# Kernel optimization log

Hardware: AMD Instinct MI355X
Metric: run time of the kernel (lower is better)

Reference implementation:

```python
import jax, jax.numpy as jnp
import numpy as np

N_WIRES = 10
N_BLOCKS = 4
BATCH = 8192
FEAT = 4 * N_WIRES
DIM = 2 ** N_WIRES
BN_EPS = 1e-5

# sign of PauliZ on wire i for each basis state index (wire 0 = most significant bit,
# matching torchquantum's [bsz, 2, 2, ..., 2] state layout)
_k = np.arange(DIM)
_bits = (_k[None, :] >> (N_WIRES - 1 - np.arange(N_WIRES))[:, None]) & 1
SIGNS = jnp.asarray(1.0 - 2.0 * _bits, dtype=jnp.float32)  # [n_wires, 2^n]

H_GATE = jnp.array([[1, 1], [1, -1]], dtype=jnp.complex64) * jnp.complex64(0.70710678)
SX_GATE = jnp.complex64(0.5) * jnp.array([[1 + 1j, 1 - 1j], [1 - 1j, 1 + 1j]], dtype=jnp.complex64)


def rx_mat(theta):
    t = jnp.asarray(theta) * 0.5
    c = jnp.cos(t).astype(jnp.complex64)
    s = (-1j) * jnp.sin(t).astype(jnp.complex64)
    return jnp.stack([jnp.stack([c, s], -1), jnp.stack([s, c], -1)], -2)


def ry_mat(theta):
    t = jnp.asarray(theta) * 0.5
    c = jnp.cos(t).astype(jnp.complex64)
    s = jnp.sin(t).astype(jnp.complex64)
    return jnp.stack([jnp.stack([c, -s], -1), jnp.stack([s, c], -1)], -2)


def rz_mat(theta):
    e = jnp.exp(jnp.complex64(-0.5j) * jnp.asarray(theta).astype(jnp.complex64))
    z = jnp.zeros_like(e)
    return jnp.stack([jnp.stack([e, z], -1), jnp.stack([z, jnp.conj(e)], -1)], -2)


def apply_1q(state, gate, wire):
    # state: [B, 2, 2, ..., 2]; gate: [2,2] (shared) or [B,2,2] (per-sample encoder)
    s = jnp.moveaxis(state, wire + 1, -1)
    if gate.ndim == 3:
        s = jnp.einsum('bij,b...j->b...i', gate, s)
    else:
        s = jnp.einsum('ij,b...j->b...i', gate, s)
    return jnp.moveaxis(s, -1, wire + 1)


def apply_cnot(state, c, t):
    s = jnp.moveaxis(state, (c + 1, t + 1), (-2, -1))  # [..., ctrl, tgt]
    s = jnp.stack([s[..., 0, :], s[..., 1, ::-1]], axis=-2)
    return jnp.moveaxis(s, (-2, -1), (c + 1, t + 1))


def measure_all_z(state):
    probs = (state.real ** 2 + state.imag ** 2).reshape(state.shape[0], -1)  # [B, 2^n]
    return probs @ SIGNS.T  # [B, n_wires]


def encode(state, feats):
    # GeneralEncoder: per wire i apply rx, ry, rz, rx with data angles feats[:, 4i..4i+3]
    for i in range(N_WIRES):
        state = apply_1q(state, rx_mat(feats[:, 4 * i]), i)
        state = apply_1q(state, ry_mat(feats[:, 4 * i + 1]), i)
        state = apply_1q(state, rz_mat(feats[:, 4 * i + 2]), i)
        state = apply_1q(state, rx_mat(feats[:, 4 * i + 3]), i)
    return state


def qnn(feats, rz1, ry1, rz2, rz3):
    B = feats.shape[0]
    state = jnp.zeros((B, DIM), jnp.complex64).at[:, 0].set(1.0)
    state = state.reshape((B,) + (2,) * N_WIRES)
    for k in range(N_BLOCKS):
        for i in range(N_WIRES):
            state = apply_1q(state, rz_mat(rz1[k, i]), i)
        for i in range(N_WIRES):
            state = apply_1q(state, ry_mat(ry1[k, i]), i)
        for i in range(N_WIRES):
            state = apply_1q(state, rz_mat(rz2[k, i]), i)
        for i in range(N_WIRES):  # circular CNOT ring
            state = apply_cnot(state, i, (i + 1) % N_WIRES)
        if k != N_BLOCKS - 1:
            state = encode(state, feats)
    outs = [measure_all_z(state)]
    for i in range(N_WIRES):
        state = apply_1q(state, H_GATE, i)
    outs.append(measure_all_z(state))
    for i in range(N_WIRES):
        state = apply_1q(state, H_GATE, i)
        state = apply_1q(state, SX_GATE, i)
    outs.append(measure_all_z(state))
    for i in range(N_WIRES):  # only the last rz3 layer is applied in the source
        state = apply_1q(state, rz_mat(rz3[-1, i]), i)
    outs.append(measure_all_z(state))
    return jnp.concatenate(outs, axis=-1)  # [B, 4*n_wires]


def setup_inputs() -> dict:
    key = jax.random.key(0)
    ks = jax.random.split(key, 13)
    pi = np.float32(np.pi)
    w_scale = 1.0 / np.sqrt(np.float32(FEAT))
    return {
        'x': jax.random.normal(ks[0], (BATCH, FEAT), jnp.float32),
        'qlin_w': jax.random.normal(ks[1], (FEAT, FEAT), jnp.float32) * w_scale,
        'qlin_b': jax.random.normal(ks[2], (FEAT,), jnp.float32) * w_scale,
        'bn_gamma': jnp.ones((FEAT,), jnp.float32),
        'bn_beta': jnp.zeros((FEAT,), jnp.float32),
        'clin_w': jax.random.normal(ks[3], (FEAT, FEAT), jnp.float32) * w_scale,
        'clin_b': jax.random.normal(ks[4], (FEAT,), jnp.float32) * w_scale,
        'lin_w': jax.random.normal(ks[5], (FEAT, 2 * FEAT), jnp.float32) * w_scale,
        'lin_b': jax.random.normal(ks[6], (FEAT,), jnp.float32) * w_scale,
        'rz1': jax.random.uniform(ks[7], (N_BLOCKS, N_WIRES), jnp.float32, -pi, pi),
        'ry1': jax.random.uniform(ks[8], (N_BLOCKS, N_WIRES), jnp.float32, -pi, pi),
        'rz2': jax.random.uniform(ks[9], (N_BLOCKS, N_WIRES), jnp.float32, -pi, pi),
        'rz3': jax.random.uniform(ks[10], (N_BLOCKS, N_WIRES), jnp.float32, -pi, pi),
    }


def reference(x, qlin_w, qlin_b, bn_gamma, bn_beta, clin_w, clin_b, lin_w, lin_b, rz1, ry1, rz2, rz3):
    # quantum branch: Linear -> BatchNorm1d (training-mode batch stats) -> QNN
    xq = x @ qlin_w.T + qlin_b
    mu = xq.mean(axis=0)
    var = ((xq - mu) ** 2).mean(axis=0)  # biased variance, as torch BN
    xq = (xq - mu) * jax.lax.rsqrt(var + BN_EPS) * bn_gamma + bn_beta
    x1 = qnn(xq, rz1, ry1, rz2, rz3)
    # classical branch
    x2 = jax.nn.relu(x @ clin_w.T + clin_b)
    return jnp.concatenate([x1, x2], axis=-1) @ lin_w.T + lin_b
```

## Files before the change

### kernel.cpp

```cpp
#include <hip/hip_runtime.h>
#include <math.h>


typedef float v2f __attribute__((ext_vector_type(2)));
typedef unsigned uiv2 __attribute__((ext_vector_type(2)));

__device__ __forceinline__ float bperm1(int addr, float v){
  return __int_as_float(__builtin_amdgcn_ds_bpermute(addr, __float_as_int(v)));
}
__device__ __forceinline__ v2f bperm2(int addr, v2f v){
  v2f r; r.x = bperm1(addr, v.x); r.y = bperm1(addr, v.y); return r;
}
__device__ __forceinline__ v2f vs(float x){ return (v2f){x,x}; }

template<int C>
__device__ __forceinline__ float dppf(float x){
  return __int_as_float(__builtin_amdgcn_update_dpp(0, __float_as_int(x),
                                                    C, 0xf, 0xf, true));
}
#define QP_X1 0xB1
#define QP_X2 0x4E

__device__ __forceinline__ float xor1f(float x, int ){ return dppf<QP_X1>(x); }
__device__ __forceinline__ float xor2f(float x, int ){ return dppf<QP_X2>(x); }

__device__ __forceinline__ float xor4f(float x, int ){
  return __int_as_float(__builtin_amdgcn_ds_swizzle(__float_as_int(x), 0x101F));
}
__device__ __forceinline__ float xor8f(float x, int ){
  return __int_as_float(__builtin_amdgcn_ds_swizzle(__float_as_int(x), 0x201F));
}

#if __has_builtin(__builtin_amdgcn_permlane16_swap) && __has_builtin(__builtin_amdgcn_permlane32_swap)
__device__ __forceinline__ float xor16f(float x, int lane){
  uiv2 r = __builtin_amdgcn_permlane16_swap(__float_as_uint(x), __float_as_uint(x),
                                            false, false);
  return __uint_as_float((lane & 16) ? r.x : r.y);
}
__device__ __forceinline__ float xor32f(float x, int lane){
  uiv2 r = __builtin_amdgcn_permlane32_swap(__float_as_uint(x), __float_as_uint(x),
                                            false, false);
  return __uint_as_float((lane & 32) ? r.x : r.y);
}
#else
__device__ __forceinline__ float xor16f(float x, int lane){ return bperm1((lane^16)<<2, x); }
__device__ __forceinline__ float xor32f(float x, int lane){ return bperm1((lane^32)<<2, x); }
#endif

#define DEF_XORV(NAME, F1) \
__device__ __forceinline__ v2f NAME(v2f v, int lane){ \
  v2f r; r.x = F1(v.x,lane); r.y = F1(v.y,lane); return r; }
DEF_XORV(xor1v,  xor1f)
DEF_XORV(xor2v,  xor2f)
DEF_XORV(xor4v,  xor4f)
DEF_XORV(xor8v,  xor8f)
DEF_XORV(xor16v, xor16f)
DEF_XORV(xor32v, xor32f)

__device__ __forceinline__ float dsum(float x){
  x += dppf<0x111>(x);
  x += dppf<0x112>(x);
  x += dppf<0x114>(x);
  x += dppf<0x118>(x);
  x += dppf<0x142>(x);
  x += dppf<0x143>(x);
  return x;
}


#define DEF_GCROSS(NAME, PFN) \
__device__ __forceinline__ void NAME(v2f (&R)[8], v2f (&I)[8], int lane, bool hi, \
                                     const float* g){ \
  const float gar = hi ? g[6] : g[0], gai = hi ? g[7] : g[1]; \
  const float gbr = hi ? g[4] : g[2], gbi = hi ? g[5] : g[3]; \
  const v2f A=vs(gar), B=vs(gai), C=vs(gbr), D=vs(gbi); \
  _Pragma("unroll") \
  for (int p=0;p<8;++p){ \
    v2f PR = PFN(R[p],lane); \
    v2f PI = PFN(I[p],lane); \
    v2f nr = A*R[p] - B*I[p] + C*PR - D*PI; \
    v2f ni = A*I[p] + B*R[p] + C*PI + D*PR; \
    R[p]=nr; I[p]=ni; } \
}
DEF_GCROSS(g_cross_x32, xor32v)
DEF_GCROSS(g_cross_x16, xor16v)
DEF_GCROSS(g_cross_x8,  xor8v)
DEF_GCROSS(g_cross_x4,  xor4v)
DEF_GCROSS(g_cross_x2,  xor2v)
DEF_GCROSS(g_cross_x1,  xor1v)

template<int PM>
__device__ __forceinline__ void g_localp(v2f (&R)[8], v2f (&I)[8], const float* g)
{
  const v2f g00r=vs(g[0]), g00i=vs(g[1]), g01r=vs(g[2]), g01i=vs(g[3]);
  const v2f g10r=vs(g[4]), g10i=vs(g[5]), g11r=vs(g[6]), g11i=vs(g[7]);
#pragma unroll
  for (int p=0;p<8;++p) if (!(p&PM)) {
    const int q = p|PM;
    v2f r0=R[p], i0=I[p], r1=R[q], i1=I[q];
    R[p] = g00r*r0 - g00i*i0 + g01r*r1 - g01i*i1;
    I[p] = g00r*i0 + g00i*r0 + g01r*i1 + g01i*r1;
    R[q] = g10r*r0 - g10i*i0 + g11r*r1 - g11i*i1;
    I[q] = g10r*i0 + g10i*r0 + g11r*i1 + g11i*r1;
  }
}

__device__ __forceinline__ void g_local9(v2f (&R)[8], v2f (&I)[8], const float* g)
{
  const v2f Gr0 = (v2f){g[0], g[4]};
  const v2f Gi0 = (v2f){g[1], g[5]};
  const v2f Gr1 = (v2f){g[2], g[6]};
  const v2f Gi1 = (v2f){g[3], g[7]};
#pragma unroll
  for (int p=0;p<8;++p) {
    v2f Rx = vs(R[p].x), Ix = vs(I[p].x);
    v2f Ry = vs(R[p].y), Iy = vs(I[p].y);
    R[p] = Gr0*Rx - Gi0*Ix + Gr1*Ry - Gi1*Iy;
    I[p] = Gr0*Ix + Gi0*Rx + Gr1*Iy + Gi1*Ry;
  }
}

__device__ __forceinline__ void cnot_ring(v2f (&R)[8], v2f (&I)[8],
                                          int addrg, int lane, bool c5)
{
#pragma unroll
  for (int p=0;p<8;++p) R[p] = bperm2(addrg, R[p]);
#pragma unroll
  for (int p=0;p<8;++p) I[p] = bperm2(addrg, I[p]);
#pragma unroll
  for (int p=0;p<4;++p) {
    v2f a=R[p], b=R[p|4];
    R[p]   = c5 ? b : a;
    R[p|4] = c5 ? a : b;
    v2f ai=I[p], bi=I[p|4];
    I[p]   = c5 ? bi : ai;
    I[p|4] = c5 ? ai : bi;
  }
#pragma unroll
  for (int p=0;p<8;++p) if ((p&4)&&!(p&2)) {
    const int q=p|2;
    v2f t=R[p]; R[p]=R[q]; R[q]=t;
    t=I[p]; I[p]=I[q]; I[q]=t;
  }
#pragma unroll
  for (int p=0;p<8;++p) if ((p&2)&&!(p&1)) {
    const int q=p|1;
    v2f t=R[p]; R[p]=R[q]; R[q]=t;
    t=I[p]; I[p]=I[q]; I[q]=t;
  }
#pragma unroll
  for (int p=1;p<8;p+=2) {
    R[p] = __builtin_shufflevector(R[p],R[p],1,0);
    I[p] = __builtin_shufflevector(I[p],I[p],1,0);
  }
#pragma unroll
  for (int p=0;p<8;++p) {
    R[p].y = xor32f(R[p].y, lane);
    I[p].y = xor32f(I[p].y, lane);
  }
}

__global__ __launch_bounds__(256) void k_pre(const float* __restrict__ x,
    const float* __restrict__ qw, const float* __restrict__ qb,
    float* __restrict__ ps)
{
  const int f = blockIdx.x >> 3, slice = blockIdx.x & 7;
  const int t = threadIdx.x;
  __shared__ float wf[40];
  __shared__ float a1[4], a2[4];
  if (t < 40) wf[t] = qw[f*40 + t];
  __syncthreads();
  const float bf = qb[f];
  float s1 = 0.f, s2 = 0.f;
#pragma unroll
  for (int i = 0; i < 4; ++i) {
    const int s = slice*1024 + t + i*256;
    const float4* xr = (const float4*)(x + s*40);
    float d = bf;
#pragma unroll
    for (int q = 0; q < 10; ++q) {
      float4 v = xr[q];
      d = fmaf(v.x, wf[4*q+0], d);
      d = fmaf(v.y, wf[4*q+1], d);
      d = fmaf(v.z, wf[4*q+2], d);
      d = fmaf(v.w, wf[4*q+3], d);
    }
    s1 += d; s2 = fmaf(d, d, s2);
  }
  s1 = dsum(s1); s2 = dsum(s2);
  const int lane = t & 63, wid = t >> 6;
  if (lane == 63) { a1[wid] = s1; a2[wid] = s2; }
  __syncthreads();
  if (t == 0) {
    ps[blockIdx.x*2+0] = a1[0]+a1[1]+a1[2]+a1[3];
    ps[blockIdx.x*2+1] = a2[0]+a2[1]+a2[2]+a2[3];
  }
}


#define GEN10(PTR) \
  g_cross_x32(R,I,lane,h0,(PTR)+0);  g_cross_x16(R,I,lane,h1,(PTR)+8);  \
  g_cross_x8 (R,I,lane,h2,(PTR)+16); g_cross_x4 (R,I,lane,h3,(PTR)+24); \
  g_cross_x2 (R,I,lane,h4,(PTR)+32); g_cross_x1 (R,I,lane,h5,(PTR)+40); \
  g_localp<4>(R,I,(PTR)+48);   g_localp<2>(R,I,(PTR)+56);   \
  g_localp<1>(R,I,(PTR)+64);   g_local9(R,I,(PTR)+72);

__global__ __launch_bounds__(256) void k_qnn(const float* __restrict__ x,
    const float* __restrict__ qlin_w, const float* __restrict__ qlin_b,
    const float* __restrict__ ps,
    const float* __restrict__ gamma, const float* __restrict__ beta,
    const float* __restrict__ rz1, const float* __restrict__ ry1,
    const float* __restrict__ rz2,
    const float* __restrict__ clin_w, const float* __restrict__ clin_b,
    const float* __restrict__ lin_w, const float* __restrict__ lin_b,
    float* __restrict__ out)
{
  const int tix  = threadIdx.x;
  const int lane = tix & 63;
  const int wv   = tix >> 6;

  __shared__ float Gbuf[40][8];
  __shared__ float bnA[40], bnC[40];
  __shared__ float Ebuf[4][10][8];
  __shared__ float Fbuf[4][3][10][8];
  __shared__ float xs [4][40];
  __shared__ float xqs[4][40];
  __shared__ float x1s[4][40];
  __shared__ float x2s[4][40];

  if (tix < 160) xs[tix/40][tix%40] = x[blockIdx.x*160 + tix];
  if (tix >= 160 && tix < 200) {
    const int gi = tix - 160;
    float g = rz1[gi], ay = ry1[gi], bz = rz2[gi];
    float ca, sa, cp, sp, cm, sm;
    sincosf(0.5f*ay, &sa, &ca);
    sincosf(0.5f*(bz+g), &sp, &cp);
    sincosf(0.5f*(bz-g), &sm, &cm);
    float* G = &Gbuf[gi][0];
    G[0]= ca*cp; G[1]=-ca*sp;
    G[2]=-sa*cm; G[3]= sa*sm;
    G[4]= sa*cm; G[5]= sa*sm;
    G[6]= ca*cp; G[7]= ca*sp;
  }
  if (tix >= 200 && tix < 240) {
    const int f = tix - 200;
    float s1 = 0.f, s2 = 0.f;
#pragma unroll
    for (int k = 0; k < 8; ++k) {
      s1 += ps[(f*8+k)*2+0];
      s2 += ps[(f*8+k)*2+1];
    }
    float mu  = s1 * (1.f/8192.f);
    float var = s2 * (1.f/8192.f) - mu*mu;
    float a = gamma[f] * rsqrtf(var + 1e-5f);
    bnA[f] = a; bnC[f] = beta[f] - mu*a;
  }
  __syncthreads();

  if (tix < 160) {
    const int sl = tix/40, f = tix - sl*40;
    const float4* qw = (const float4*)(qlin_w + f*40);
    float acc = qlin_b[f];
#pragma unroll
    for (int q = 0; q < 10; ++q) {
      float4 v = qw[q];
      acc = fmaf(v.x, xs[sl][4*q+0], acc);
      acc = fmaf(v.y, xs[sl][4*q+1], acc);
      acc = fmaf(v.z, xs[sl][4*q+2], acc);
      acc = fmaf(v.w, xs[sl][4*q+3], acc);
    }
    xqs[sl][f] = acc;
  }
  __syncthreads();

  if (lane < 10) {
    const int i = lane;
    const int f = 4*i;
    float h0 = 0.5f * fmaf(xqs[wv][f+0], bnA[f+0], bnC[f+0]);
    float h1 = 0.5f * fmaf(xqs[wv][f+1], bnA[f+1], bnC[f+1]);
    float h2 = 0.5f * fmaf(xqs[wv][f+2], bnA[f+2], bnC[f+2]);
    float h3 = 0.5f * fmaf(xqs[wv][f+3], bnA[f+3], bnC[f+3]);
    float c0,s0,c1,s1,c2,s2,c3,s3;
    sincosf(h0,&s0,&c0); sincosf(h1,&s1,&c1);
    sincosf(h2,&s2,&c2); sincosf(h3,&s3,&c3);
    float A00r=c1*c0, A00i= s1*s0;
    float A01r=-s1*c0, A01i=-c1*s0;
    float A10r= s1*c0, A10i=-c1*s0;
    float A11r= c1*c0, A11i=-s1*s0;
    float B00r = A00r*c2 + A00i*s2, B00i = A00i*c2 - A00r*s2;
    float B01r = A01r*c2 + A01i*s2, B01i = A01i*c2 - A01r*s2;
    float B10r = A10r*c2 - A10i*s2, B10i = A10i*c2 + A10r*s2;
    float B11r = A11r*c2 - A11i*s2, B11i = A11i*c2 + A11r*s2;
    float* e = &Ebuf[wv][i][0];
    e[0] = c3*B00r + s3*B10i;  e[1] = c3*B00i - s3*B10r;
    e[2] = c3*B01r + s3*B11i;  e[3] = c3*B01i - s3*B11r;
    e[4] = c3*B10r + s3*B00i;  e[5] = c3*B10i - s3*B00r;
    e[6] = c3*B11r + s3*B01i;  e[7] = c3*B11i - s3*B01r;
  }

  if (lane < 30) {
    const int k = lane/10, i = lane - k*10;
    const float* U = &Gbuf[(k+1)*10 + i][0];
    const float* E = &Ebuf[wv][i][0];
    float u00r=U[0],u00i=U[1],u01r=U[2],u01i=U[3],u10r=U[4],u10i=U[5],u11r=U[6],u11i=U[7];
    float e00r=E[0],e00i=E[1],e01r=E[2],e01i=E[3],e10r=E[4],e10i=E[5],e11r=E[6],e11i=E[7];
    float* F = &Fbuf[wv][k][i][0];
    F[0] = u00r*e00r - u00i*e00i + u01r*e10r - u01i*e10i;
    F[1] = u00r*e00i + u00i*e00r + u01r*e10i + u01i*e10r;
    F[2] = u00r*e01r - u00i*e01i + u01r*e11r - u01i*e11i;
    F[3] = u00r*e01i + u00i*e01r + u01r*e11i + u01i*e11r;
    F[4] = u10r*e00r - u10i*e00i + u11r*e10r - u11i*e10i;
    F[5] = u10r*e00i + u10i*e00r + u11r*e10i + u11i*e10r;
    F[6] = u10r*e01r - u10i*e01i + u11r*e11r - u11i*e11i;
    F[7] = u10r*e01i + u10i*e01r + u11r*e11i + u11i*e11r;
  }

  const bool h0 = (lane & 32) != 0;
  const bool h1 = (lane & 16) != 0;
  const bool h2 = (lane &  8) != 0;
  const bool h3 = (lane &  4) != 0;
  const bool h4 = (lane &  2) != 0;
  const bool h5 = (lane &  1) != 0;
  const int addrg = (lane ^ (lane >> 1)) << 2;

  v2f R[8], I[8];
  {
    const int l0=lane&1, l1=(lane>>1)&1, l2=(lane>>2)&1,
              l3=(lane>>3)&1, l4=(lane>>4)&1, l5=(lane>>5)&1;
    float csr, csi;
    {
      int b = l3^l4; csr = Gbuf[2][4*b]; csi = Gbuf[2][4*b+1];
      b = l2^l3; float gr=Gbuf[3][4*b], gi=Gbuf[3][4*b+1];
      float tr = csr*gr - csi*gi, ti = csr*gi + csi*gr; csr=tr; csi=ti;
      b = l1^l2; gr=Gbuf[4][4*b]; gi=Gbuf[4][4*b+1];
      tr = csr*gr - csi*gi; ti = csr*gi + csi*gr; csr=tr; csi=ti;
      b = l0^l1; gr=Gbuf[5][4*b]; gi=Gbuf[5][4*b+1];
      tr = csr*gr - csi*gi; ti = csr*gi + csi*gr; csr=tr; csi=ti;
    }
    float cer,cei,cor_,coi;
    {
      const int b5 = l5, b4 = l4^l5;
      float ar = Gbuf[0][4*b5],     ai = Gbuf[0][4*b5+1];
      float br = Gbuf[1][4*b4],     bi = Gbuf[1][4*b4+1];
      float tr = ar*br - ai*bi,     ti = ar*bi + ai*br;
      cer = tr*csr - ti*csi;  cei = tr*csi + ti*csr;
      ar = Gbuf[0][4*(1^b5)]; ai = Gbuf[0][4*(1^b5)+1];
      br = Gbuf[1][4*(1^b4)]; bi = Gbuf[1][4*(1^b4)+1];
      tr = ar*br - ai*bi;     ti = ar*bi + ai*br;
      cor_ = tr*csr - ti*csi; coi = tr*csi + ti*csr;
    }
    float p67r[4], p67i[4], p89r[4], p89i[4];
#pragma unroll
    for (int b6=0;b6<2;++b6)
#pragma unroll
      for (int b7=0;b7<2;++b7) {
        const float x6r = Gbuf[6][4*b6], x6i = Gbuf[6][4*b6+1];
        const float x7r = Gbuf[7][4*b7], x7i = Gbuf[7][4*b7+1];
        p67r[b6*2+b7] = x6r*x7r - x6i*x7i;
        p67i[b6*2+b7] = x6r*x7i + x6i*x7r;
      }
#pragma unroll
    for (int b8=0;b8<2;++b8)
#pragma unroll
      for (int b9=0;b9<2;++b9) {
        const float x8r = Gbuf[8][4*b8], x8i = Gbuf[8][4*b8+1];
        const float x9r = Gbuf[9][4*b9], x9i = Gbuf[9][4*b9+1];
        p89r[b8*2+b9] = x8r*x9r - x8i*x9i;
        p89i[b8*2+b9] = x8r*x9i + x8i*x9r;
      }
    float ter[4], tei[4], tor_[4], toi[4];
#pragma unroll
    for (int m=0;m<4;++m) {
      ter[m]  = cer*p67r[m] - cei*p67i[m];
      tei[m]  = cer*p67i[m] + cei*p67r[m];
      tor_[m] = cor_*p67r[m] - coi*p67i[m];
      toi[m]  = cor_*p67i[m] + coi*p67r[m];
    }
#pragma unroll
    for (int p=0;p<8;++p) {
      const int b3 = (p>>2)&1, b2 = (p>>1)&1, b1 = p&1;
      const int i67 = ((b3 ^ l0) << 1) | (b2 ^ b3);
      const int b1p = b1 ^ b2;
      const int ix  = (b1p<<1) | b1;
      const int iy  = (b1p<<1) | (1^b1);
      R[p].x = ter[i67]*p89r[ix] - tei[i67]*p89i[ix];
      I[p].x = ter[i67]*p89i[ix] + tei[i67]*p89r[ix];
      R[p].y = tor_[i67]*p89r[iy] - toi[i67]*p89i[iy];
      I[p].y = tor_[i67]*p89i[iy] + toi[i67]*p89r[iy];
    }
  }

  { const float* F = &Fbuf[wv][0][0][0]; GEN10(F) }
  cnot_ring(R,I,addrg,lane,h5);
  { const float* F = &Fbuf[wv][1][0][0]; GEN10(F) }
  cnot_ring(R,I,addrg,lane,h5);
  { const float* F = &Fbuf[wv][2][0][0]; GEN10(F) }
  cnot_ring(R,I,addrg,lane,h5);

  float* dst = &x1s[wv][0];

  {
    v2f pv[8];
#pragma unroll
    for (int p=0;p<8;++p) pv[p] = R[p]*R[p] + I[p]*I[p];
    v2f T8 = (pv[0]-pv[1]) + (pv[2]-pv[3]) + (pv[4]-pv[5]) + (pv[6]-pv[7]);
    v2f aa[4];
#pragma unroll
    for (int m=0;m<4;++m) aa[m] = pv[2*m] + pv[2*m+1];
    v2f T7 = (aa[0]-aa[1]) + (aa[2]-aa[3]);
    v2f T6 = (aa[0]+aa[1]) - (aa[2]+aa[3]);
    v2f S  = (aa[0]+aa[1]) + (aa[2]+aa[3]);
    float q8 = T8.x + T8.y;
    float q7 = T7.x + T7.y;
    float q6 = T6.x + T6.y;
    float q9 = S.x - S.y;
    float P  = S.x + S.y;

    float v = P;
    { float pt = xor1f (v,lane); v = h5 ? (pt - v) : (pt + v); }
    { float pt = xor2f (v,lane); v = h4 ? (pt - v) : (pt + v); }
    { float pt = xor4f (v,lane); v = h3 ? (pt - v) : (pt + v); }
    { float pt = xor8f (v,lane); v = h2 ? (pt - v) : (pt + v); }
    { float pt = xor16f(v,lane); v = h1 ? (pt - v) : (pt + v); }
    { float pt = xor32f(v,lane); v = h0 ? (pt - v) : (pt + v); }

    q6 = dsum(q6); q7 = dsum(q7); q8 = dsum(q8); q9 = dsum(q9);

    if (lane==32) dst[0]=v;
    if (lane==16) dst[1]=v;
    if (lane== 8) dst[2]=v;
    if (lane== 4) dst[3]=v;
    if (lane== 2) dst[4]=v;
    if (lane== 1) dst[5]=v;
    if (lane==63){ dst[6]=q6; dst[7]=q7; dst[8]=q8; dst[9]=q9; }
  }

#define XYC(PFN,HW,W) { \
    v2f U=vs(0.f), V=vs(0.f); \
    _Pragma("unroll") \
    for (int p=0;p<8;++p) { \
      v2f PR = PFN(R[p],lane); \
      v2f PI = PFN(I[p],lane); \
      U += R[p]*PR + I[p]*PI; \
      V += I[p]*PR - R[p]*PI; \
    } \
    float u = U.x + U.y; \
    float vv = V.x + V.y; \
    vv = (HW) ? vv : -vv; \
    u = dsum(u); vv = dsum(vv); \
    if (lane==63){ dst[10+(W)]=u; dst[20+(W)]=vv; dst[30+(W)]=vv; } \
  }
  XYC(xor32v,h0,0) XYC(xor16v,h1,1) XYC(xor8v,h2,2)
  XYC(xor4v ,h3,3) XYC(xor2v ,h4,4) XYC(xor1v,h5,5)
#undef XYC

#define XYL(PM,W) { \
    v2f U=vs(0.f), V=vs(0.f); \
    _Pragma("unroll") \
    for (int p=0;p<8;++p) if (!(p&(PM))) { \
      const int q=p|(PM); \
      U += R[p]*R[q] + I[p]*I[q]; \
      V += I[p]*R[q] - R[p]*I[q]; \
    } \
    float u = U.x + U.y; \
    float vv = V.x + V.y; \
    u = dsum(u); vv = dsum(vv); \
    if (lane==63){ dst[10+(W)]=2.f*u; float y=-2.f*vv; dst[20+(W)]=y; dst[30+(W)]=y; } \
  }
  XYL(4,6) XYL(2,7) XYL(1,8)
#undef XYL

  {
    float u=0.f, vv=0.f;
#pragma unroll
    for (int p=0;p<8;++p) {
      u  = fmaf(R[p].x, R[p].y, u);  u  = fmaf(I[p].x, I[p].y, u);
      vv = fmaf(I[p].x, R[p].y, vv); vv = fmaf(-R[p].x, I[p].y, vv);
    }
    u = dsum(u); vv = dsum(vv);
    if (lane==63){ dst[19]=2.f*u; float y=-2.f*vv; dst[29]=y; dst[39]=y; }
  }

  __syncthreads();
  if (tix < 160) {
    const int sl = tix/40, f = tix - sl*40;
    const float4* cw = (const float4*)(clin_w + f*40);
    float acc = clin_b[f];
#pragma unroll
    for (int q = 0; q < 10; ++q) {
      float4 v = cw[q];
      acc = fmaf(v.x, xs[sl][4*q+0], acc);
      acc = fmaf(v.y, xs[sl][4*q+1], acc);
      acc = fmaf(v.z, xs[sl][4*q+2], acc);
      acc = fmaf(v.w, xs[sl][4*q+3], acc);
    }
    x2s[sl][f] = fmaxf(acc, 0.f);
  }
  __syncthreads();
  if (tix < 160) {
    const int sl = tix/40, f = tix - sl*40;
    const float4* lw = (const float4*)(lin_w + f*80);
    float o = lin_b[f];
#pragma unroll
    for (int q = 0; q < 10; ++q) {
      float4 v = lw[q];
      o = fmaf(v.x, x1s[sl][4*q+0], o);
      o = fmaf(v.y, x1s[sl][4*q+1], o);
      o = fmaf(v.z, x1s[sl][4*q+2], o);
      o = fmaf(v.w, x1s[sl][4*q+3], o);
    }
#pragma unroll
    for (int q = 10; q < 20; ++q) {
      float4 v = lw[q];
      o = fmaf(v.x, x2s[sl][4*(q-10)+0], o);
      o = fmaf(v.y, x2s[sl][4*(q-10)+1], o);
      o = fmaf(v.z, x2s[sl][4*(q-10)+2], o);
      o = fmaf(v.w, x2s[sl][4*(q-10)+3], o);
    }
    out[blockIdx.x*160 + tix] = o;
  }
}

extern "C" void kernel_launch(void* const* d_in, const int* in_sizes, int n_in,
                              void* d_out, int out_size, void* d_ws, size_t ws_size,
                              hipStream_t stream)
{
  const float* x      = (const float*)d_in[0];
  const float* qlin_w = (const float*)d_in[1];
  const float* qlin_b = (const float*)d_in[2];
  const float* bn_g   = (const float*)d_in[3];
  const float* bn_b   = (const float*)d_in[4];
  const float* clin_w = (const float*)d_in[5];
  const float* clin_b = (const float*)d_in[6];
  const float* lin_w  = (const float*)d_in[7];
  const float* lin_b  = (const float*)d_in[8];
  const float* rz1    = (const float*)d_in[9];
  const float* ry1    = (const float*)d_in[10];
  const float* rz2    = (const float*)d_in[11];

  float* ps  = (float*)d_ws;
  float* out = (float*)d_out;

  hipLaunchKernelGGL(k_pre, dim3(320),  dim3(256), 0, stream, x, qlin_w, qlin_b, ps);
  hipLaunchKernelGGL(k_qnn, dim3(2048), dim3(256), 0, stream,
                     x, qlin_w, qlin_b, ps, bn_g, bn_b, rz1, ry1, rz2,
                     clin_w, clin_b, lin_w, lin_b, out);
}
```

Before: 166.4 us.

## Process two samples per wavefront with interleaved state vectors and fast trig

Each wavefront now holds two independent 1024-amplitude state vectors, one per sample, and interleaves their gate, CNOT-ring and measurement work. Each block therefore covers eight samples and the grid is halved. The independent instruction streams are meant to hide the latency of the bpermute and DPP shuffles, and the per-block setup of gate matrices and batch-norm constants is amortized over twice as many samples. sincosf is also replaced by __sinf/__cosf. The trade-offs are roughly double the state registers per thread, which may lower occupancy, and slightly reduced trig accuracy.

```diff
diff --git a/kernel.cpp b/kernel.cpp
--- a/kernel.cpp
+++ b/kernel.cpp
@@ -120,6 +120,21 @@
   }
 }
 
+__device__ __forceinline__ void gen10(v2f (&R)[8], v2f (&I)[8], int lane,
+    bool h0, bool h1, bool h2, bool h3, bool h4, bool h5, const float* F)
+{
+  g_cross_x32(R,I,lane,h0,F+0);
+  g_cross_x16(R,I,lane,h1,F+8);
+  g_cross_x8 (R,I,lane,h2,F+16);
+  g_cross_x4 (R,I,lane,h3,F+24);
+  g_cross_x2 (R,I,lane,h4,F+32);
+  g_cross_x1 (R,I,lane,h5,F+40);
+  g_localp<4>(R,I,F+48);
+  g_localp<2>(R,I,F+56);
+  g_localp<1>(R,I,F+64);
+  g_local9(R,I,F+72);
+}
+
 __device__ __forceinline__ void cnot_ring(v2f (&R)[8], v2f (&I)[8],
                                           int addrg, int lane, bool c5)
 {
@@ -197,13 +212,6 @@
   }
 }
 
-
-#define GEN10(PTR) \
-  g_cross_x32(R,I,lane,h0,(PTR)+0);  g_cross_x16(R,I,lane,h1,(PTR)+8);  \
-  g_cross_x8 (R,I,lane,h2,(PTR)+16); g_cross_x4 (R,I,lane,h3,(PTR)+24); \
-  g_cross_x2 (R,I,lane,h4,(PTR)+32); g_cross_x1 (R,I,lane,h5,(PTR)+40); \
-  g_localp<4>(R,I,(PTR)+48);   g_localp<2>(R,I,(PTR)+56);   \
-  g_localp<1>(R,I,(PTR)+64);   g_local9(R,I,(PTR)+72);
 
 __global__ __launch_bounds__(256) void k_qnn(const float* __restrict__ x,
     const float* __restrict__ qlin_w, const float* __restrict__ qlin_b,
@@ -218,24 +226,28 @@
   const int tix  = threadIdx.x;
   const int lane = tix & 63;
   const int wv   = tix >> 6;
+  const int ll   = lane & 31;
+  const int hw   = lane >> 5;
+  const int smp  = wv*2 + hw;
 
   __shared__ float Gbuf[40][8];
   __shared__ float bnA[40], bnC[40];
-  __shared__ float Ebuf[4][10][8];
-  __shared__ float Fbuf[4][3][10][8];
-  __shared__ float xs [4][40];
-  __shared__ float xqs[4][40];
-  __shared__ float x1s[4][40];
-  __shared__ float x2s[4][40];
-
-  if (tix < 160) xs[tix/40][tix%40] = x[blockIdx.x*160 + tix];
+  __shared__ float Ebuf[8][10][8];
+  __shared__ float Fbuf[8][3][10][8];
+  __shared__ float xs [8][40];
+  __shared__ float xqs[8][40];
+  __shared__ float x1s[8][40];
+  __shared__ float x2s[8][40];
+
+  ((float*)xs)[tix] = x[blockIdx.x*320 + tix];
+  if (tix < 64) ((float*)xs)[256 + tix] = x[blockIdx.x*320 + 256 + tix];
   if (tix >= 160 && tix < 200) {
     const int gi = tix - 160;
     float g = rz1[gi], ay = ry1[gi], bz = rz2[gi];
-    float ca, sa, cp, sp, cm, sm;
-    sincosf(0.5f*ay, &sa, &ca);
-    sincosf(0.5f*(bz+g), &sp, &cp);
-    sincosf(0.5f*(bz-g), &sm, &cm);
+    float ha = 0.5f*ay, hp = 0.5f*(bz+g), hm = 0.5f*(bz-g);
+    float ca = __cosf(ha), sa = __sinf(ha);
+    float cp = __cosf(hp), sp = __sinf(hp);
+    float cm = __cosf(hm), sm = __sinf(hm);
     float* G = &Gbuf[gi][0];
     G[0]= ca*cp; G[1]=-ca*sp;
     G[2]=-sa*cm; G[3]= sa*sm;
@@ -257,8 +269,9 @@
   }
   __syncthreads();
 
-  if (tix < 160) {
-    const int sl = tix/40, f = tix - sl*40;
+#pragma unroll
+  for (int r = 0; r < 2; ++r) if (tix < 160) {
+    const int sl = r*4 + tix/40, f = tix - (tix/40)*40;
     const float4* qw = (const float4*)(qlin_w + f*40);
     float acc = qlin_b[f];
 #pragma unroll
@@ -273,16 +286,17 @@
   }
   __syncthreads();
 
-  if (lane < 10) {
-    const int i = lane;
+  if (ll < 10) {
+    const int i = ll;
     const int f = 4*i;
-    float h0 = 0.5f * fmaf(xqs[wv][f+0], bnA[f+0], bnC[f+0]);
-    float h1 = 0.5f * fmaf(xqs[wv][f+1], bnA[f+1], bnC[f+1]);
-    float h2 = 0.5f * fmaf(xqs[wv][f+2], bnA[f+2], bnC[f+2]);
-    float h3 = 0.5f * fmaf(xqs[wv][f+3], bnA[f+3], bnC[f+3]);
-    float c0,s0,c1,s1,c2,s2,c3,s3;
-    sincosf(h0,&s0,&c0); sincosf(h1,&s1,&c1);
-    sincosf(h2,&s2,&c2); sincosf(h3,&s3,&c3);
+    float a0 = 0.5f * fmaf(xqs[smp][f+0], bnA[f+0], bnC[f+0]);
+    float a1 = 0.5f * fmaf(xqs[smp][f+1], bnA[f+1], bnC[f+1]);
+    float a2 = 0.5f * fmaf(xqs[smp][f+2], bnA[f+2], bnC[f+2]);
+    float a3 = 0.5f * fmaf(xqs[smp][f+3], bnA[f+3], bnC[f+3]);
+    float c0 = __cosf(a0), s0 = __sinf(a0);
+    float c1 = __cosf(a1), s1 = __sinf(a1);
+    float c2 = __cosf(a2), s2 = __sinf(a2);
+    float c3 = __cosf(a3), s3 = __sinf(a3);
     float A00r=c1*c0, A00i= s1*s0;
     float A01r=-s1*c0, A01i=-c1*s0;
     float A10r= s1*c0, A10i=-c1*s0;
@@ -291,20 +305,20 @@
     float B01r = A01r*c2 + A01i*s2, B01i = A01i*c2 - A01r*s2;
     float B10r = A10r*c2 - A10i*s2, B10i = A10i*c2 + A10r*s2;
     float B11r = A11r*c2 - A11i*s2, B11i = A11i*c2 + A11r*s2;
-    float* e = &Ebuf[wv][i][0];
+    float* e = &Ebuf[smp][i][0];
     e[0] = c3*B00r + s3*B10i;  e[1] = c3*B00i - s3*B10r;
     e[2] = c3*B01r + s3*B11i;  e[3] = c3*B01i - s3*B11r;
     e[4] = c3*B10r + s3*B00i;  e[5] = c3*B10i - s3*B00r;
     e[6] = c3*B11r + s3*B01i;  e[7] = c3*B11i - s3*B01r;
   }
 
-  if (lane < 30) {
-    const int k = lane/10, i = lane - k*10;
+  if (ll < 30) {
+    const int k = ll/10, i = ll - k*10;
     const float* U = &Gbuf[(k+1)*10 + i][0];
-    const float* E = &Ebuf[wv][i][0];
+    const float* E = &Ebuf[smp][i][0];
     float u00r=U[0],u00i=U[1],u01r=U[2],u01i=U[3],u10r=U[4],u10i=U[5],u11r=U[6],u11i=U[7];
     float e00r=E[0],e00i=E[1],e01r=E[2],e01i=E[3],e10r=E[4],e10i=E[5],e11r=E[6],e11i=E[7];
-    float* F = &Fbuf[wv][k][i][0];
+    float* F = &Fbuf[smp][k][i][0];
     F[0] = u00r*e00r - u00i*e00i + u01r*e10r - u01i*e10i;
     F[1] = u00r*e00i + u00i*e00r + u01r*e10i + u01i*e10r;
     F[2] = u00r*e01r - u00i*e01i + u01r*e11r - u01i*e11i;
@@ -323,7 +337,7 @@
   const bool h5 = (lane &  1) != 0;
   const int addrg = (lane ^ (lane >> 1)) << 2;
 
-  v2f R[8], I[8];
+  v2f R[2][8], I[2][8];
   {
     const int l0=lane&1, l1=(lane>>1)&1, l2=(lane>>2)&1,
               l3=(lane>>3)&1, l4=(lane>>4)&1, l5=(lane>>5)&1;
@@ -368,14 +382,6 @@
         p89r[b8*2+b9] = x8r*x9r - x8i*x9i;
         p89i[b8*2+b9] = x8r*x9i + x8i*x9r;
       }
-    float ter[4], tei[4], tor_[4], toi[4];
-#pragma unroll
-    for (int m=0;m<4;++m) {
-      ter[m]  = cer*p67r[m] - cei*p67i[m];
-      tei[m]  = cer*p67i[m] + cei*p67r[m];
-      tor_[m] = cor_*p67r[m] - coi*p67i[m];
-      toi[m]  = cor_*p67i[m] + coi*p67r[m];
-    }
 #pragma unroll
     for (int p=0;p<8;++p) {
       const int b3 = (p>>2)&1, b2 = (p>>1)&1, b1 = p&1;
@@ -383,66 +389,82 @@
       const int b1p = b1 ^ b2;
       const int ix  = (b1p<<1) | b1;
       const int iy  = (b1p<<1) | (1^b1);
-      R[p].x = ter[i67]*p89r[ix] - tei[i67]*p89i[ix];
-      I[p].x = ter[i67]*p89i[ix] + tei[i67]*p89r[ix];
-      R[p].y = tor_[i67]*p89r[iy] - toi[i67]*p89i[iy];
-      I[p].y = tor_[i67]*p89i[iy] + toi[i67]*p89r[iy];
-    }
-  }
-
-  { const float* F = &Fbuf[wv][0][0][0]; GEN10(F) }
-  cnot_ring(R,I,addrg,lane,h5);
-  { const float* F = &Fbuf[wv][1][0][0]; GEN10(F) }
-  cnot_ring(R,I,addrg,lane,h5);
-  { const float* F = &Fbuf[wv][2][0][0]; GEN10(F) }
-  cnot_ring(R,I,addrg,lane,h5);
-
-  float* dst = &x1s[wv][0];
-
-  {
-    v2f pv[8];
-#pragma unroll
-    for (int p=0;p<8;++p) pv[p] = R[p]*R[p] + I[p]*I[p];
-    v2f T8 = (pv[0]-pv[1]) + (pv[2]-pv[3]) + (pv[4]-pv[5]) + (pv[6]-pv[7]);
-    v2f aa[4];
-#pragma unroll
-    for (int m=0;m<4;++m) aa[m] = pv[2*m] + pv[2*m+1];
-    v2f T7 = (aa[0]-aa[1]) + (aa[2]-aa[3]);
-    v2f T6 = (aa[0]+aa[1]) - (aa[2]+aa[3]);
-    v2f S  = (aa[0]+aa[1]) + (aa[2]+aa[3]);
-    float q8 = T8.x + T8.y;
-    float q7 = T7.x + T7.y;
-    float q6 = T6.x + T6.y;
-    float q9 = S.x - S.y;
-    float P  = S.x + S.y;
-
-    float v = P;
-    { float pt = xor1f (v,lane); v = h5 ? (pt - v) : (pt + v); }
-    { float pt = xor2f (v,lane); v = h4 ? (pt - v) : (pt + v); }
-    { float pt = xor4f (v,lane); v = h3 ? (pt - v) : (pt + v); }
-    { float pt = xor8f (v,lane); v = h2 ? (pt - v) : (pt + v); }
-    { float pt = xor16f(v,lane); v = h1 ? (pt - v) : (pt + v); }
-    { float pt = xor32f(v,lane); v = h0 ? (pt - v) : (pt + v); }
-
-    q6 = dsum(q6); q7 = dsum(q7); q8 = dsum(q8); q9 = dsum(q9);
-
-    if (lane==32) dst[0]=v;
-    if (lane==16) dst[1]=v;
-    if (lane== 8) dst[2]=v;
-    if (lane== 4) dst[3]=v;
-    if (lane== 2) dst[4]=v;
-    if (lane== 1) dst[5]=v;
-    if (lane==63){ dst[6]=q6; dst[7]=q7; dst[8]=q8; dst[9]=q9; }
-  }
+      const float ter = cer*p67r[i67] - cei*p67i[i67];
+      const float tei = cer*p67i[i67] + cei*p67r[i67];
+      const float tor_ = cor_*p67r[i67] - coi*p67i[i67];
+      const float toi  = cor_*p67i[i67] + coi*p67r[i67];
+      R[0][p].x = ter*p89r[ix] - tei*p89i[ix];
+      I[0][p].x = ter*p89i[ix] + tei*p89r[ix];
+      R[0][p].y = tor_*p89r[iy] - toi*p89i[iy];
+      I[0][p].y = tor_*p89i[iy] + toi*p89r[iy];
+    }
+  }
+#pragma unroll
+  for (int p=0;p<8;++p) { R[1][p] = R[0][p]; I[1][p] = I[0][p]; }
+
+#pragma unroll
+  for (int s=0;s<2;++s) gen10(R[s],I[s],lane,h0,h1,h2,h3,h4,h5,&Fbuf[2*wv+s][0][0][0]);
+#pragma unroll
+  for (int s=0;s<2;++s) cnot_ring(R[s],I[s],addrg,lane,h5);
+#pragma unroll
+  for (int s=0;s<2;++s) gen10(R[s],I[s],lane,h0,h1,h2,h3,h4,h5,&Fbuf[2*wv+s][1][0][0]);
+#pragma unroll
+  for (int s=0;s<2;++s) cnot_ring(R[s],I[s],addrg,lane,h5);
+#pragma unroll
+  for (int s=0;s<2;++s) gen10(R[s],I[s],lane,h0,h1,h2,h3,h4,h5,&Fbuf[2*wv+s][2][0][0]);
+#pragma unroll
+  for (int s=0;s<2;++s) cnot_ring(R[s],I[s],addrg,lane,h5);
+
+#pragma unroll
+  for (int s=0;s<2;++s) {
+    v2f (&Rr)[8] = R[s];
+    v2f (&Ir)[8] = I[s];
+    float* dst = &x1s[2*wv + s][0];
+
+    {
+      v2f pv[8];
+#pragma unroll
+      for (int p=0;p<8;++p) pv[p] = Rr[p]*Rr[p] + Ir[p]*Ir[p];
+      v2f T8 = (pv[0]-pv[1]) + (pv[2]-pv[3]) + (pv[4]-pv[5]) + (pv[6]-pv[7]);
+      v2f aa[4];
+#pragma unroll
+      for (int m=0;m<4;++m) aa[m] = pv[2*m] + pv[2*m+1];
+      v2f T7 = (aa[0]-aa[1]) + (aa[2]-aa[3]);
+      v2f T6 = (aa[0]+aa[1]) - (aa[2]+aa[3]);
+      v2f S  = (aa[0]+aa[1]) + (aa[2]+aa[3]);
+      float q8 = T8.x + T8.y;
+      float q7 = T7.x + T7.y;
+      float q6 = T6.x + T6.y;
+      float q9 = S.x - S.y;
+      float P  = S.x + S.y;
+
+      float v = P;
+      { float pt = xor1f (v,lane); v = h5 ? (pt - v) : (pt + v); }
+      { float pt = xor2f (v,lane); v = h4 ? (pt - v) : (pt + v); }
+      { float pt = xor4f (v,lane); v = h3 ? (pt - v) : (pt + v); }
+      { float pt = xor8f (v,lane); v = h2 ? (pt - v) : (pt + v); }
+      { float pt = xor16f(v,lane); v = h1 ? (pt - v) : (pt + v); }
+      { float pt = xor32f(v,lane); v = h0 ? (pt - v) : (pt + v); }
+
+      q6 = dsum(q6); q7 = dsum(q7); q8 = dsum(q8); q9 = dsum(q9);
+
+      if (lane==32) dst[0]=v;
+      if (lane==16) dst[1]=v;
+      if (lane== 8) dst[2]=v;
+      if (lane== 4) dst[3]=v;
+      if (lane== 2) dst[4]=v;
+      if (lane== 1) dst[5]=v;
+      if (lane==63){ dst[6]=q6; dst[7]=q7; dst[8]=q8; dst[9]=q9; }
+    }
 
 #define XYC(PFN,HW,W) { \
     v2f U=vs(0.f), V=vs(0.f); \
     _Pragma("unroll") \
     for (int p=0;p<8;++p) { \
-      v2f PR = PFN(R[p],lane); \
-      v2f PI = PFN(I[p],lane); \
-      U += R[p]*PR + I[p]*PI; \
-      V += I[p]*PR - R[p]*PI; \
+      v2f PR = PFN(Rr[p],lane); \
+      v2f PI = PFN(Ir[p],lane); \
+      U += Rr[p]*PR + Ir[p]*PI; \
+      V += Ir[p]*PR - Rr[p]*PI; \
     } \
     float u = U.x + U.y; \
     float vv = V.x + V.y; \
@@ -450,8 +472,8 @@
     u = dsum(u); vv = dsum(vv); \
     if (lane==63){ dst[10+(W)]=u; dst[20+(W)]=vv; dst[30+(W)]=vv; } \
   }
-  XYC(xor32v,h0,0) XYC(xor16v,h1,1) XYC(xor8v,h2,2)
-  XYC(xor4v ,h3,3) XYC(xor2v ,h4,4) XYC(xor1v,h5,5)
+    XYC(xor32v,h0,0) XYC(xor16v,h1,1) XYC(xor8v,h2,2)
+    XYC(xor4v ,h3,3) XYC(xor2v ,h4,4) XYC(xor1v,h5,5)
 #undef XYC
 
 #define XYL(PM,W) { \
@@ -459,31 +481,33 @@
     _Pragma("unroll") \
     for (int p=0;p<8;++p) if (!(p&(PM))) { \
       const int q=p|(PM); \
-      U += R[p]*R[q] + I[p]*I[q]; \
-      V += I[p]*R[q] - R[p]*I[q]; \
+      U += Rr[p]*Rr[q] + Ir[p]*Ir[q]; \
+      V += Ir[p]*Rr[q] - Rr[p]*Ir[q]; \
     } \
     float u = U.x + U.y; \
     float vv = V.x + V.y; \
     u = dsum(u); vv = dsum(vv); \
     if (lane==63){ dst[10+(W)]=2.f*u; float y=-2.f*vv; dst[20+(W)]=y; dst[30+(W)]=y; } \
   }
-  XYL(4,6) XYL(2,7) XYL(1,8)
+    XYL(4,6) XYL(2,7) XYL(1,8)
 #undef XYL
 
-  {
-    float u=0.f, vv=0.f;
-#pragma unroll
-    for (int p=0;p<8;++p) {
-      u  = fmaf(R[p].x, R[p].y, u);  u  = fmaf(I[p].x, I[p].y, u);
-      vv = fmaf(I[p].x, R[p].y, vv); vv = fmaf(-R[p].x, I[p].y, vv);
-    }
-    u = dsum(u); vv = dsum(vv);
-    if (lane==63){ dst[19]=2.f*u; float y=-2.f*vv; dst[29]=y; dst[39]=y; }
+    {
+      float u=0.f, vv=0.f;
+#pragma unroll
+      for (int p=0;p<8;++p) {
+        u  = fmaf(Rr[p].x, Rr[p].y, u);  u  = fmaf(Ir[p].x, Ir[p].y, u);
+        vv = fmaf(Ir[p].x, Rr[p].y, vv); vv = fmaf(-Rr[p].x, Ir[p].y, vv);
+      }
+      u = dsum(u); vv = dsum(vv);
+      if (lane==63){ dst[19]=2.f*u; float y=-2.f*vv; dst[29]=y; dst[39]=y; }
+    }
   }
 
   __syncthreads();
-  if (tix < 160) {
-    const int sl = tix/40, f = tix - sl*40;
+#pragma unroll
+  for (int r = 0; r < 2; ++r) if (tix < 160) {
+    const int sl = r*4 + tix/40, f = tix - (tix/40)*40;
     const float4* cw = (const float4*)(clin_w + f*40);
     float acc = clin_b[f];
 #pragma unroll
@@ -497,8 +521,9 @@
     x2s[sl][f] = fmaxf(acc, 0.f);
   }
   __syncthreads();
-  if (tix < 160) {
-    const int sl = tix/40, f = tix - sl*40;
+#pragma unroll
+  for (int r = 0; r < 2; ++r) if (tix < 160) {
+    const int sl = r*4 + tix/40, f = tix - (tix/40)*40;
     const float4* lw = (const float4*)(lin_w + f*80);
     float o = lin_b[f];
 #pragma unroll
@@ -517,7 +542,7 @@
       o = fmaf(v.z, x2s[sl][4*(q-10)+2], o);
       o = fmaf(v.w, x2s[sl][4*(q-10)+3], o);
     }
-    out[blockIdx.x*160 + tix] = o;
+    out[blockIdx.x*320 + r*160 + tix] = o;
   }
 }
 
@@ -542,7 +567,7 @@
   float* out = (float*)d_out;
 
   hipLaunchKernelGGL(k_pre, dim3(320),  dim3(256), 0, stream, x, qlin_w, qlin_b, ps);
-  hipLaunchKernelGGL(k_qnn, dim3(2048), dim3(256), 0, stream,
+  hipLaunchKernelGGL(k_qnn, dim3(1024), dim3(256), 0, stream,
                      x, qlin_w, qlin_b, ps, bn_g, bn_b, rz1, ry1, rz2,
                      clin_w, clin_b, lin_w, lin_b, out);
 }
```

Result: slower. 181.1 us (+8.9%).
